# Optimization experiments

Hardware: AMD Instinct MI355X
Metric: run time of the kernel (lower is better)

Reference implementation:

```python
import jax, jax.numpy as jnp
import numpy as np

N_HOST = 50000
N_FLOW = 200000
D = 128
D_OUT = 32
E = 1_000_000
L = 2


def setup_inputs() -> dict:
    key = jax.random.key(0)
    ks = jax.random.split(key, 12)
    s = 0.05  # keep activations well-scaled across layers
    return {
        "x_host": jax.random.normal(ks[0], (N_HOST, D), jnp.float32),
        "x_flow": jax.random.normal(ks[1], (N_FLOW, D), jnp.float32),
        "ehf_src": jax.random.randint(ks[2], (E,), 0, N_HOST),
        "ehf_dst": jax.random.randint(ks[3], (E,), 0, N_FLOW),
        "efh_src": jax.random.randint(ks[4], (E,), 0, N_FLOW),
        "efh_dst": jax.random.randint(ks[5], (E,), 0, N_HOST),
        "Wl": jax.random.normal(ks[6], (L, 2, D, D), jnp.float32) * s,
        "bl": jax.random.normal(ks[7], (L, 2, D), jnp.float32) * s,
        "Wr": jax.random.normal(ks[8], (L, 2, D, D), jnp.float32) * s,
        "br": jax.random.normal(ks[9], (L, 2, D), jnp.float32) * s,
        "W_out": jax.random.normal(ks[10], (D, D_OUT), jnp.float32) * s,
        "b_out": jax.random.normal(ks[11], (D_OUT,), jnp.float32) * s,
    }


def _sage(x_src, x_dst, src, dst, n_dst, wl, bll, wr, brr):
    # SAGEConv (bipartite, mean aggr): lin_l(mean_{j->i} x_src[j]) + lin_r(x_dst[i])
    msg = x_src[src]                                         # [E, D] gather
    agg = jax.ops.segment_sum(msg, dst, num_segments=n_dst)  # [n_dst, D] scatter-add
    cnt = jax.ops.segment_sum(jnp.ones((src.shape[0], 1), x_src.dtype), dst,
                              num_segments=n_dst)
    mean = agg / jnp.maximum(cnt, 1.0)
    return mean @ wl + bll + x_dst @ wr + brr


def reference(x_host, x_flow, ehf_src, ehf_dst, efh_src, efh_dst,
              Wl, bl, Wr, br, W_out, b_out):
    h, f = x_host, x_flow
    for l in range(L):
        # ('host','to','flow') -> updates flow; ('flow','to','host') -> updates host
        nf = _sage(h, f, ehf_src, ehf_dst, N_FLOW, Wl[l, 0], bl[l, 0], Wr[l, 0], br[l, 0])
        nh = _sage(f, h, efh_src, efh_dst, N_HOST, Wl[l, 1], bl[l, 1], Wr[l, 1], br[l, 1])
        f = jax.nn.leaky_relu(nf)  # negative_slope 0.01, matches F.leaky_relu default
        h = jax.nn.leaky_relu(nh)
    return f @ W_out + b_out
```

## Files before the change

### kernel.cpp

```cpp
#include <hip/hip_runtime.h>
#include <stdint.h>

#define N_HOST 50000
#define N_FLOW 200000
#define DIM 128
#define DOUTN 32
#define NEDGE 1000000
#define NLAYER 2

#define GSH_F 8
#define GSH_H 6
#define NB_F ((N_FLOW + (1 << GSH_F) - 1) >> GSH_F)
#define NB_H ((N_HOST + (1 << GSH_H) - 1) >> GSH_H)
#define BCAP 2048
#define AST 136

#define CAST_FBLK 25000
#define CAST_HBLK 6250
#define ZOFF  (CAST_FBLK + CAST_HBLK)
#define ZBLK  13
#define RW_OFF (ZOFF + ZBLK)
#define RO_OFF (RW_OFF + 64)
#define PREP_GRID (RO_OFF + 2)

typedef __bf16 bf16;
typedef __bf16 bf16x4 __attribute__((ext_vector_type(4)));
typedef __bf16 bf16x8 __attribute__((ext_vector_type(8)));
typedef float floatx2 __attribute__((ext_vector_type(2)));
typedef float floatx4 __attribute__((ext_vector_type(4)));
typedef int intx4 __attribute__((ext_vector_type(4)));

__global__ __launch_bounds__(256)
void prep_all_k(const float* __restrict__ xf, const float* __restrict__ xh,
                const float* __restrict__ Wl, const float* __restrict__ Wr,
                const float* __restrict__ Wo,
                bf16* __restrict__ fA, bf16* __restrict__ hAB,
                int* __restrict__ bcnt2,
                bf16* __restrict__ WlF, bf16* __restrict__ WrF,
                bf16* __restrict__ WoF) {
    int bid = blockIdx.x;
    int t = threadIdx.x;
    if (bid < CAST_FBLK) {
        int i = (bid * 256 + t) * 4;
        float4 v = *(const float4*)(xf + i);
        bf16x4 o;
        o[0] = (bf16)v.x; o[1] = (bf16)v.y; o[2] = (bf16)v.z; o[3] = (bf16)v.w;
        *(bf16x4*)(fA + i) = o;
    } else if (bid < ZOFF) {
        int i = ((bid - CAST_FBLK) * 256 + t) * 4;
        float4 v = *(const float4*)(xh + i);
        bf16x4 o;
        o[0] = (bf16)v.x; o[1] = (bf16)v.y; o[2] = (bf16)v.z; o[3] = (bf16)v.w;
        int row = i >> 7, col = i & 127;
        *(bf16x4*)(hAB + row * 256 + col) = o;
    } else if (bid < RW_OFF) {
        int base = (bid - ZOFF) * 2048;
#pragma unroll
        for (int j = 0; j < 8; ++j) {
            int i = base + j * 256 + t;
            if (i < (NB_F + NB_H) * 16) bcnt2[i] = 0;
        }
    } else if (bid < RO_OFF) {
        int b = bid - RW_OFF;
        int y = b >> 3;
        int x = b & 7;
        int lane = t & 63;
        int w = x * 4 + (t >> 6);
        int ct = w >> 2, k0q = w & 3;
        int quad = lane >> 4, m = lane & 15;
        int mat = y & 3;
        const float* W = (y < 4 ? Wl : Wr) + (size_t)mat * DIM * DIM;
        bf16* out = (y < 4 ? WlF : WrF) + (size_t)mat * DIM * DIM;
        bf16x8 o;
#pragma unroll
        for (int j = 0; j < 8; ++j) o[j] = (bf16)W[(k0q * 32 + quad * 8 + j) * DIM + ct * 16 + m];
        *(bf16x8*)(out + ((ct * 4 + k0q) * 64 + lane) * 8) = o;
    } else {
        int b2 = bid - RO_OFF;
        int lane = t & 63;
        int w = b2 * 4 + (t >> 6);
        int ct = w >> 2, k0q = w & 3;
        int quad = lane >> 4, m = lane & 15;
        bf16x8 o;
#pragma unroll
        for (int j = 0; j < 8; ++j) o[j] = (bf16)Wo[(k0q * 32 + quad * 8 + j) * DOUTN + ct * 16 + m];
        *(bf16x8*)(WoF + ((ct * 4 + k0q) * 64 + lane) * 8) = o;
    }
}

__global__ __launch_bounds__(256)
void bucket_scatter2_k(const int* __restrict__ sF, const int* __restrict__ dF,
                       const int* __restrict__ sH, const int* __restrict__ dH,
                       int* bcntF, int* bcntH,
                       int* __restrict__ bkF, int* __restrict__ bkH) {
    int dir = blockIdx.y;
    const int* src = dir ? sH : sF;
    const int* dst = dir ? dH : dF;
    int* bcnt = dir ? bcntH : bcntF;
    int* bkey = dir ? bkH : bkF;
    int gsh = dir ? GSH_H : GSH_F;
    int e = blockIdx.x * 256 + threadIdx.x;
    if (e < NEDGE) {
        int d = dst[e];
        int b = d >> gsh;
        int p = atomicAdd(&bcnt[b << 4], 1);
        if (p < BCAP) bkey[(b << 11) + p] = (src[e] << 8) | (d & ((1 << gsh) - 1));
    }
}

__global__ __launch_bounds__(256)
void bucket_sort2_k(const int* __restrict__ bcntF, const int* __restrict__ bcntH,
                    const int* __restrict__ bkF, const int* __restrict__ bkH,
                    int2* __restrict__ rsF2, int2* __restrict__ rsH2,
                    int* __restrict__ esF, int* __restrict__ esH) {
    __shared__ int cnts[256];
    __shared__ int sd[256];
    __shared__ int ldsout[BCAP];
    int dir = blockIdx.y;
    const int* bcnt = dir ? bcntH : bcntF;
    const int* bkey = dir ? bkH : bkF;
    int2* rs2 = dir ? rsH2 : rsF2;
    int* es = dir ? esH : esF;
    int gsh = dir ? GSH_H : GSH_F;
    int b = blockIdx.x, t = threadIdx.x;
    int G = 1 << gsh;
    int base = b << 11;
    int cnt = bcnt[b << 4];
    if (cnt > BCAP) cnt = BCAP;
    int keys[8]; int nk = 0;
    for (int i = t; i < cnt; i += 256) keys[nk++] = bkey[base + i];
    cnts[t] = 0;
    __syncthreads();
    for (int j = 0; j < nk; ++j) atomicAdd(&cnts[keys[j] & 255], 1);
    __syncthreads();
    int v = cnts[t];
    int x = v;
    sd[t] = x; __syncthreads();
    for (int o = 1; o < 256; o <<= 1) {
        int y = (t >= o) ? sd[t - o] : 0;
        __syncthreads();
        x += y; sd[t] = x; __syncthreads();
    }
    int ex = x - v;
    if (t < G) rs2[(b << gsh) + t] = make_int2(base + ex, base + ex + v);
    cnts[t] = ex;
    __syncthreads();
    for (int j = 0; j < nk; ++j) {
        int k = keys[j];
        int p = atomicAdd(&cnts[k & 255], 1);
        ldsout[p] = k >> 8;
    }
    __syncthreads();
    for (int i = t; i < cnt; i += 256) es[base + i] = ldsout[i];
}

__device__ __forceinline__ void acc_pk4(floatx2* acc, intx4 v) {
    uint32_t d[4] = {(uint32_t)v.x, (uint32_t)v.y, (uint32_t)v.z, (uint32_t)v.w};
#pragma unroll
    for (int k = 0; k < 4; ++k) {
        floatx2 u;
        u.x = __uint_as_float(d[k] << 16);
        u.y = __uint_as_float(d[k] & 0xffff0000u);
        asm("v_pk_add_f32 %0, %1, %0" : "+v"(acc[k]) : "v"(u));
    }
}

#define LRELU(v) ((v) > 0.f ? (v) : 0.01f * (v))

__global__ __launch_bounds__(512, 8)
void host_fused(const int2* __restrict__ rs2, const int* __restrict__ csr,
                const intx4* __restrict__ x4,
                const bf16* __restrict__ hA,
                const bf16* __restrict__ W1f, const bf16* __restrict__ W2f,
                const float* __restrict__ b1, const float* __restrict__ b2,
                bf16* __restrict__ hB) {
    __shared__ __align__(16) bf16 TM[64 * AST];
    int t = threadIdx.x;
    int row0 = blockIdx.x << 6;
    {
        int q = t >> 4, c = t & 15;
#pragma unroll
        for (int p = 0; p < 2; ++p) {
            int lr = p * 32 + q;
            int r = row0 + lr;
            floatx2 a2[4];
#pragma unroll
            for (int k = 0; k < 4; ++k) a2[k] = (floatx2){0.f, 0.f};
            float inv = 1.0f;
            if (r < N_HOST) {
                int2 se = rs2[r];
                int s0 = se.x, s1 = se.y;
                for (int e = s0; e < s1; ++e) {
                    int s = csr[e];
                    intx4 v = x4[s * 16 + c];
                    acc_pk4(a2, v);
                }
                int deg = s1 - s0;
                inv = 1.0f / (float)(deg > 0 ? deg : 1);
            }
            bf16x8 o;
#pragma unroll
            for (int k = 0; k < 4; ++k) {
                o[2 * k]     = (bf16)(a2[k].x * inv);
                o[2 * k + 1] = (bf16)(a2[k].y * inv);
            }
            *(bf16x8*)(TM + lr * AST + c * 8) = o;
        }
    }
    __syncthreads();
    int lane = t & 63, wv = t >> 6;
    int quad = lane >> 4, m = lane & 15;
    int ccol = wv * 16 + m;
    floatx4 zero4 = {0.f, 0.f, 0.f, 0.f};
    floatx4 acc[4];
#pragma unroll
    for (int rt = 0; rt < 4; ++rt) acc[rt] = zero4;
    {
        bf16x8 B[4];
#pragma unroll
        for (int k = 0; k < 4; ++k)
            B[k] = *(const bf16x8*)(W1f + ((wv * 4 + k) * 64 + lane) * 8);
#pragma unroll
        for (int rt = 0; rt < 4; ++rt)
#pragma unroll
            for (int k = 0; k < 4; ++k) {
                bf16x8 a = *(const bf16x8*)(TM + (rt * 16 + m) * AST + quad * 8 + k * 32);
                acc[rt] = __builtin_amdgcn_mfma_f32_16x16x32_bf16(a, B[k], acc[rt], 0, 0, 0);
            }
#pragma unroll
        for (int k = 0; k < 4; ++k)
            B[k] = *(const bf16x8*)(W2f + ((wv * 4 + k) * 64 + lane) * 8);
#pragma unroll
        for (int rt = 0; rt < 4; ++rt) {
            int ar = row0 + rt * 16 + m;
            if (ar >= N_HOST) ar = 0;
#pragma unroll
            for (int k = 0; k < 4; ++k) {
                bf16x8 a = *(const bf16x8*)(hA + (size_t)ar * 256 + quad * 8 + k * 32);
                acc[rt] = __builtin_amdgcn_mfma_f32_16x16x32_bf16(a, B[k], acc[rt], 0, 0, 0);
            }
        }
    }
    float bias = b1[ccol] + b2[ccol];
#pragma unroll
    for (int rt = 0; rt < 4; ++rt)
#pragma unroll
        for (int r4 = 0; r4 < 4; ++r4) {
            int row = row0 + rt * 16 + quad * 4 + r4;
            if (row < N_HOST) {
                float v0 = acc[rt][r4] + bias;
                hB[(size_t)row * 256 + ccol] = (bf16)LRELU(v0);
            }
        }
}

__global__ __launch_bounds__(512, 8)
void flow_fused(const int2* __restrict__ rs2, const int* __restrict__ csr,
                const intx4* __restrict__ tab,
                const bf16* __restrict__ fA,
                const bf16* __restrict__ Wl0f, const bf16* __restrict__ Wr0f,
                const bf16* __restrict__ Wl2f, const bf16* __restrict__ Wr2f,
                const float* __restrict__ bl0, const float* __restrict__ br0,
                const float* __restrict__ bl2, const float* __restrict__ br2,
                const bf16* __restrict__ Wof, const float* __restrict__ bo,
                float* __restrict__ outf) {
    __shared__ __align__(16) bf16 T0[64 * AST];
    __shared__ __align__(16) bf16 T1[64 * AST];
    int t = threadIdx.x;
    int row0 = blockIdx.x << 6;
    {
        int q = t >> 4, c = t & 15;
#pragma unroll
        for (int p = 0; p < 2; ++p) {
            int lr = p * 32 + q;
            int r = row0 + lr;
            int2 se = rs2[r];
            int s0 = se.x, s1 = se.y;
            floatx2 a2[4], b2[4];
#pragma unroll
            for (int k = 0; k < 4; ++k) { a2[k] = (floatx2){0.f, 0.f}; b2[k] = (floatx2){0.f, 0.f}; }
            for (int e = s0; e < s1; ++e) {
                int sa = csr[e];
                intx4 va = tab[sa * 32 + c];
                intx4 vb = tab[sa * 32 + 16 + c];
                acc_pk4(a2, va); acc_pk4(b2, vb);
            }
            int deg = s1 - s0;
            float inv = 1.0f / (float)(deg > 0 ? deg : 1);
            bf16x8 oa, ob;
#pragma unroll
            for (int k = 0; k < 4; ++k) {
                oa[2 * k]     = (bf16)(a2[k].x * inv);
                oa[2 * k + 1] = (bf16)(a2[k].y * inv);
                ob[2 * k]     = (bf16)(b2[k].x * inv);
                ob[2 * k + 1] = (bf16)(b2[k].y * inv);
            }
            *(bf16x8*)(T0 + lr * AST + c * 8) = oa;
            *(bf16x8*)(T1 + lr * AST + c * 8) = ob;
        }
    }
    __syncthreads();
    int lane = t & 63, wv = t >> 6;
    int quad = lane >> 4, m = lane & 15;
    int ccol = wv * 16 + m;
    floatx4 zero4 = {0.f, 0.f, 0.f, 0.f};
    floatx4 acc[4];
#pragma unroll
    for (int rt = 0; rt < 4; ++rt) acc[rt] = zero4;
    {
        bf16x8 B[4];
#pragma unroll
        for (int k = 0; k < 4; ++k)
            B[k] = *(const bf16x8*)(Wl0f + ((wv * 4 + k) * 64 + lane) * 8);
#pragma unroll
        for (int rt = 0; rt < 4; ++rt)
#pragma unroll
            for (int k = 0; k < 4; ++k) {
                bf16x8 a = *(const bf16x8*)(T0 + (rt * 16 + m) * AST + quad * 8 + k * 32);
                acc[rt] = __builtin_amdgcn_mfma_f32_16x16x32_bf16(a, B[k], acc[rt], 0, 0, 0);
            }
#pragma unroll
        for (int k = 0; k < 4; ++k)
            B[k] = *(const bf16x8*)(Wr0f + ((wv * 4 + k) * 64 + lane) * 8);
#pragma unroll
        for (int rt = 0; rt < 4; ++rt)
#pragma unroll
            for (int k = 0; k < 4; ++k) {
                bf16x8 a = *(const bf16x8*)(fA + (size_t)(row0 + rt * 16 + m) * DIM + quad * 8 + k * 32);
                acc[rt] = __builtin_amdgcn_mfma_f32_16x16x32_bf16(a, B[k], acc[rt], 0, 0, 0);
            }
    }
    {
        float bias = bl0[ccol] + br0[ccol];
        __syncthreads();
#pragma unroll
        for (int rt = 0; rt < 4; ++rt)
#pragma unroll
            for (int r4 = 0; r4 < 4; ++r4) {
                int lr = rt * 16 + quad * 4 + r4;
                float v0 = acc[rt][r4] + bias;
                T0[lr * AST + ccol] = (bf16)LRELU(v0);
            }
        __syncthreads();
    }
#pragma unroll
    for (int rt = 0; rt < 4; ++rt) acc[rt] = zero4;
    {
        bf16x8 B[4];
#pragma unroll
        for (int k = 0; k < 4; ++k)
            B[k] = *(const bf16x8*)(Wl2f + ((wv * 4 + k) * 64 + lane) * 8);
#pragma unroll
        for (int rt = 0; rt < 4; ++rt)
#pragma unroll
            for (int k = 0; k < 4; ++k) {
                bf16x8 a = *(const bf16x8*)(T1 + (rt * 16 + m) * AST + quad * 8 + k * 32);
                acc[rt] = __builtin_amdgcn_mfma_f32_16x16x32_bf16(a, B[k], acc[rt], 0, 0, 0);
            }
#pragma unroll
        for (int k = 0; k < 4; ++k)
            B[k] = *(const bf16x8*)(Wr2f + ((wv * 4 + k) * 64 + lane) * 8);
#pragma unroll
        for (int rt = 0; rt < 4; ++rt)
#pragma unroll
            for (int k = 0; k < 4; ++k) {
                bf16x8 a = *(const bf16x8*)(T0 + (rt * 16 + m) * AST + quad * 8 + k * 32);
                acc[rt] = __builtin_amdgcn_mfma_f32_16x16x32_bf16(a, B[k], acc[rt], 0, 0, 0);
            }
    }
    {
        float bias = bl2[ccol] + br2[ccol];
        __syncthreads();
#pragma unroll
        for (int rt = 0; rt < 4; ++rt)
#pragma unroll
            for (int r4 = 0; r4 < 4; ++r4) {
                int lr = rt * 16 + quad * 4 + r4;
                float v0 = acc[rt][r4] + bias;
                T1[lr * AST + ccol] = (bf16)LRELU(v0);
            }
        __syncthreads();
    }
    {
        int s = wv >> 1, h = wv & 1;
        bf16x8 BO[4];
#pragma unroll
        for (int k = 0; k < 4; ++k)
            BO[k] = *(const bf16x8*)(Wof + ((h * 4 + k) * 64 + lane) * 8);
        floatx4 o = zero4;
        const bf16* fp = T1 + (s * 16 + m) * AST + quad * 8;
#pragma unroll
        for (int k = 0; k < 4; ++k) {
            bf16x8 af = *(const bf16x8*)(fp + k * 32);
            o = __builtin_amdgcn_mfma_f32_16x16x32_bf16(af, BO[k], o, 0, 0, 0);
        }
        float bov = bo[h * 16 + m];
#pragma unroll
        for (int r = 0; r < 4; ++r) {
            int row = row0 + s * 16 + quad * 4 + r;
            outf[row * DOUTN + h * 16 + m] = o[r] + bov;
        }
    }
}

extern "C" void kernel_launch(void* const* d_in, const int* in_sizes, int n_in,
                              void* d_out, int out_size, void* d_ws, size_t ws_size,
                              hipStream_t stream) {
    (void)in_sizes; (void)n_in; (void)out_size; (void)ws_size;
    const float* x_host  = (const float*)d_in[0];
    const float* x_flow  = (const float*)d_in[1];
    const int*   ehf_src = (const int*)d_in[2];
    const int*   ehf_dst = (const int*)d_in[3];
    const int*   efh_src = (const int*)d_in[4];
    const int*   efh_dst = (const int*)d_in[5];
    const float* Wl      = (const float*)d_in[6];
    const float* bl      = (const float*)d_in[7];
    const float* Wr      = (const float*)d_in[8];
    const float* br      = (const float*)d_in[9];
    const float* W_out   = (const float*)d_in[10];
    const float* b_out   = (const float*)d_in[11];
    float* out = (float*)d_out;

    char* basep = (char*)d_ws;
    size_t off = 0;
    auto alloc = [&](size_t b) -> void* {
        void* p = basep + off;
        off += (b + 255) & ~(size_t)255;
        return p;
    };

    bf16* fA     = (bf16*)alloc((size_t)N_FLOW * DIM * 2);
    bf16* hAB    = (bf16*)alloc((size_t)N_HOST * 256 * 2);
    bf16* WlF    = (bf16*)alloc((size_t)NLAYER * 2 * DIM * DIM * 2);
    bf16* WrF    = (bf16*)alloc((size_t)NLAYER * 2 * DIM * DIM * 2);
    bf16* WoF    = (bf16*)alloc((size_t)DIM * DOUTN * 2);

    int* bcnt2   = (int*)alloc((size_t)(NB_F + NB_H) * 16 * 4);
    int* bcntF   = bcnt2;
    int* bcntH   = bcnt2 + NB_F * 16;
    int* bkF     = (int*)alloc((size_t)NB_F * BCAP * 4);
    int* bkH     = (int*)alloc((size_t)NB_H * BCAP * 4);
    int* esF     = (int*)alloc((size_t)NB_F * BCAP * 4);
    int* esH     = (int*)alloc((size_t)NB_H * BCAP * 4);
    int2* rsF2   = (int2*)alloc((size_t)NB_F * (1 << GSH_F) * 8);
    int2* rsH2   = (int2*)alloc((size_t)NB_H * (1 << GSH_H) * 8);

    prep_all_k<<<PREP_GRID, 256, 0, stream>>>(
        x_flow, x_host, Wl, Wr, W_out, fA, hAB, bcnt2, WlF, WrF, WoF);

    bucket_scatter2_k<<<dim3((NEDGE + 255) / 256, 2), 256, 0, stream>>>(
        ehf_src, ehf_dst, efh_src, efh_dst, bcntF, bcntH, bkF, bkH);

    bucket_sort2_k<<<dim3(NB_F, 2), 256, 0, stream>>>(
        bcntF, bcntH, bkF, bkH, rsF2, rsH2, esF, esH);

    host_fused<<<(N_HOST + 63) / 64, 512, 0, stream>>>(
        rsH2, esH, (const intx4*)fA, hAB,
        WlF + 1 * DIM * DIM, WrF + 1 * DIM * DIM,
        bl + 1 * DIM, br + 1 * DIM, hAB + 128);

    flow_fused<<<N_FLOW / 64, 512, 0, stream>>>(
        rsF2, esF, (const intx4*)hAB, fA,
        WlF + 0 * DIM * DIM, WrF + 0 * DIM * DIM,
        WlF + 2 * DIM * DIM, WrF + 2 * DIM * DIM,
        bl + 0 * DIM, br + 0 * DIM, bl + 2 * DIM, br + 2 * DIM,
        WoF, b_out, out);
}
```

Before: 507.6 us.

## Shrink host_fused tile to 16 rows and split each row's edges across two lane groups

The host-layer fused kernel now handles 16 rows per block instead of 64, launching four times as many blocks. Each row's neighbor gather is split between two 16-lane halves that take alternating edges, are unrolled by two for more loads in flight, and are combined with a cross-lane shuffle. The aim is more parallelism and memory-level concurrency in the gather, which is latency-bound for the long host in-degree lists (about 20 edges per row). In exchange each block does less MFMA work per weight load, reloading the weight fragments four times as often, and bounds checks are dropped because 50000 divides evenly by 16.

```diff
diff --git a/kernel.cpp b/kernel.cpp
--- a/kernel.cpp
+++ b/kernel.cpp
@@ -174,84 +174,79 @@
                 const bf16* __restrict__ W1f, const bf16* __restrict__ W2f,
                 const float* __restrict__ b1, const float* __restrict__ b2,
                 bf16* __restrict__ hB) {
-    __shared__ __align__(16) bf16 TM[64 * AST];
+    __shared__ __align__(16) bf16 TM[16 * AST];
     int t = threadIdx.x;
-    int row0 = blockIdx.x << 6;
-    {
-        int q = t >> 4, c = t & 15;
-#pragma unroll
-        for (int p = 0; p < 2; ++p) {
-            int lr = p * 32 + q;
-            int r = row0 + lr;
-            floatx2 a2[4];
-#pragma unroll
-            for (int k = 0; k < 4; ++k) a2[k] = (floatx2){0.f, 0.f};
-            float inv = 1.0f;
-            if (r < N_HOST) {
-                int2 se = rs2[r];
-                int s0 = se.x, s1 = se.y;
-                for (int e = s0; e < s1; ++e) {
-                    int s = csr[e];
-                    intx4 v = x4[s * 16 + c];
-                    acc_pk4(a2, v);
-                }
-                int deg = s1 - s0;
-                inv = 1.0f / (float)(deg > 0 ? deg : 1);
-            }
+    int lane = t & 63, wv = t >> 6;
+    int row0 = blockIdx.x << 4;
+    {
+        int c = lane & 15;
+        int q = lane >> 4;
+        int half = q & 1;
+        int sub = q >> 1;
+        int r = row0 + wv * 2 + sub;
+        int2 se = rs2[r];
+        floatx2 a2[4];
+#pragma unroll
+        for (int k = 0; k < 4; ++k) a2[k] = (floatx2){0.f, 0.f};
+        int e = se.x + half;
+        for (; e + 2 < se.y; e += 4) {
+            int s0 = csr[e], s1 = csr[e + 2];
+            intx4 v0 = x4[s0 * 16 + c];
+            intx4 v1 = x4[s1 * 16 + c];
+            acc_pk4(a2, v0); acc_pk4(a2, v1);
+        }
+        if (e < se.y) {
+            int s = csr[e];
+            intx4 v = x4[s * 16 + c];
+            acc_pk4(a2, v);
+        }
+#pragma unroll
+        for (int k = 0; k < 4; ++k) {
+            a2[k].x += __shfl_xor(a2[k].x, 16, 64);
+            a2[k].y += __shfl_xor(a2[k].y, 16, 64);
+        }
+        if (half == 0) {
+            int deg = se.y - se.x;
+            float inv = 1.0f / (float)(deg > 0 ? deg : 1);
             bf16x8 o;
 #pragma unroll
             for (int k = 0; k < 4; ++k) {
                 o[2 * k]     = (bf16)(a2[k].x * inv);
                 o[2 * k + 1] = (bf16)(a2[k].y * inv);
             }
-            *(bf16x8*)(TM + lr * AST + c * 8) = o;
-        }
-    }
-    __syncthreads();
-    int lane = t & 63, wv = t >> 6;
+            *(bf16x8*)(TM + (wv * 2 + sub) * AST + c * 8) = o;
+        }
+    }
+    __syncthreads();
     int quad = lane >> 4, m = lane & 15;
     int ccol = wv * 16 + m;
-    floatx4 zero4 = {0.f, 0.f, 0.f, 0.f};
-    floatx4 acc[4];
-#pragma unroll
-    for (int rt = 0; rt < 4; ++rt) acc[rt] = zero4;
+    floatx4 acc = {0.f, 0.f, 0.f, 0.f};
     {
         bf16x8 B[4];
 #pragma unroll
         for (int k = 0; k < 4; ++k)
             B[k] = *(const bf16x8*)(W1f + ((wv * 4 + k) * 64 + lane) * 8);
 #pragma unroll
-        for (int rt = 0; rt < 4; ++rt)
-#pragma unroll
-            for (int k = 0; k < 4; ++k) {
-                bf16x8 a = *(const bf16x8*)(TM + (rt * 16 + m) * AST + quad * 8 + k * 32);
-                acc[rt] = __builtin_amdgcn_mfma_f32_16x16x32_bf16(a, B[k], acc[rt], 0, 0, 0);
-            }
+        for (int k = 0; k < 4; ++k) {
+            bf16x8 a = *(const bf16x8*)(TM + m * AST + quad * 8 + k * 32);
+            acc = __builtin_amdgcn_mfma_f32_16x16x32_bf16(a, B[k], acc, 0, 0, 0);
+        }
 #pragma unroll
         for (int k = 0; k < 4; ++k)
             B[k] = *(const bf16x8*)(W2f + ((wv * 4 + k) * 64 + lane) * 8);
 #pragma unroll
-        for (int rt = 0; rt < 4; ++rt) {
-            int ar = row0 + rt * 16 + m;
-            if (ar >= N_HOST) ar = 0;
-#pragma unroll
-            for (int k = 0; k < 4; ++k) {
-                bf16x8 a = *(const bf16x8*)(hA + (size_t)ar * 256 + quad * 8 + k * 32);
-                acc[rt] = __builtin_amdgcn_mfma_f32_16x16x32_bf16(a, B[k], acc[rt], 0, 0, 0);
-            }
+        for (int k = 0; k < 4; ++k) {
+            bf16x8 a = *(const bf16x8*)(hA + (size_t)(row0 + m) * 256 + quad * 8 + k * 32);
+            acc = __builtin_amdgcn_mfma_f32_16x16x32_bf16(a, B[k], acc, 0, 0, 0);
         }
     }
     float bias = b1[ccol] + b2[ccol];
 #pragma unroll
-    for (int rt = 0; rt < 4; ++rt)
-#pragma unroll
-        for (int r4 = 0; r4 < 4; ++r4) {
-            int row = row0 + rt * 16 + quad * 4 + r4;
-            if (row < N_HOST) {
-                float v0 = acc[rt][r4] + bias;
-                hB[(size_t)row * 256 + ccol] = (bf16)LRELU(v0);
-            }
-        }
+    for (int r4 = 0; r4 < 4; ++r4) {
+        int row = row0 + quad * 4 + r4;
+        float v0 = acc[r4] + bias;
+        hB[(size_t)row * 256 + ccol] = (bf16)LRELU(v0);
+    }
 }
 
 __global__ __launch_bounds__(512, 8)
@@ -454,7 +449,7 @@
     bucket_sort2_k<<<dim3(NB_F, 2), 256, 0, stream>>>(
         bcntF, bcntH, bkF, bkH, rsF2, rsH2, esF, esH);
 
-    host_fused<<<(N_HOST + 63) / 64, 512, 0, stream>>>(
+    host_fused<<<N_HOST / 16, 512, 0, stream>>>(
         rsH2, esH, (const intx4*)fA, hAB,
         WlF + 1 * DIM * DIM, WrF + 1 * DIM * DIM,
         bl + 1 * DIM, br + 1 * DIM, hAB + 128);
```

Measured after the change: 499.5 us. No clear change (-1.6%).
